# Optimization experiments

Hardware: AMD Instinct MI355X
Metric: run time of the kernel (lower is better)

Reference implementation:

```python
import jax, jax.numpy as jnp
import numpy as np

B, N = 8192, 200  # batch of patches, fixed 200 points per patch


def setup_inputs() -> dict:
    key = jax.random.key(0)
    k1, = jax.random.split(key, 1)
    network_in = jax.random.normal(k1, (B, N, 13), dtype=jnp.float32)
    # learned parameters per build(): outward_shift init 0.25, a init 1, b init 0
    outward_shift = jnp.full((1,), 0.25, dtype=jnp.float32)
    a = jnp.ones((1,), dtype=jnp.float32)
    b = jnp.zeros((1,), dtype=jnp.float32)
    return {"network_in": network_in, "outward_shift": outward_shift, "a": a, "b": b}


def reference(network_in, outward_shift, a, b):
    w = network_in[:, :, 0:1]          # [B,N,1]
    xyz1 = network_in[:, :, 1:4]
    xyz2 = network_in[:, :, 4:7]       # also orig_xyz2
    norm1 = network_in[:, :, 7:10]
    norm2 = network_in[:, :, 10:13]

    w = jax.nn.relu(a * w + b) + 1e-8  # [B,N,1]

    v1 = xyz1 + norm1 * outward_shift
    v2 = xyz2 + norm2 * outward_shift

    w_sum = jnp.sum(w, axis=1)                       # [B,1]
    v1_ctr = jnp.sum(v1 * w, axis=1) / w_sum         # [B,3]
    v2_ctr = jnp.sum(v2 * w, axis=1) / w_sum         # [B,3]
    v1 = v1 - v1_ctr[:, None, :]
    v2 = v2 - v2_ctr[:, None, :]

    # cov = v2^T diag(w) v1, done without materializing the NxN diagonal
    cov = jnp.einsum('bni,bn,bnj->bij', v2, w[:, :, 0], v1)  # [B,3,3]

    # tf.linalg.svd: cov = u diag(s) v^T  ->  jnp svd: cov = u diag(s) vh, v = vh^T
    u, s, vh = jnp.linalg.svd(cov)
    v = jnp.swapaxes(vh, -1, -2)

    VUt = jnp.einsum('bik,bjk->bij', v, u)           # v @ u^T
    det_VUt = jnp.linalg.det(VUt)                    # [B]
    ones = jnp.ones_like(det_VUt)
    d = jnp.stack([ones, ones, det_VUt], axis=-1)    # [B,3]

    # R = v @ diag([1,1,det]) @ u^T
    R = jnp.einsum('bik,bk,bjk->bij', v, d, u)       # [B,3,3]

    t = v1_ctr - jnp.einsum('bij,bj->bi', R, v2_ctr) # [B,3]
    new_coords = jnp.einsum('bij,bnj->bni', R, xyz2) + t[:, None, :]
    return new_coords
```

## Files before the change

### kernel.cpp

```cpp
#include <hip/hip_runtime.h>
#include <math.h>

#define NPTS 200
#define NCH  13
#define BLK  256
#define FPB  (NPTS * NCH)

typedef float f4u __attribute__((ext_vector_type(4), aligned(4)));

typedef struct { float x, y, z; } f3s;

#define ACCUMULATE(Q0,Q1,Q2,Q3,Q4,Q5,Q6,Q7,Q8,Q9,Q10,Q11,Q12)               \
    {                                                                        \
        float wt = aa * (Q0) + bb;                                           \
        wt = fmaxf(wt, 0.f) + 1e-8f;                                         \
        const float v1x = fmaf(shift, (Q7),  (Q1));                          \
        const float v1y = fmaf(shift, (Q8),  (Q2));                          \
        const float v1z = fmaf(shift, (Q9),  (Q3));                          \
        const float v2x = fmaf(shift, (Q10), (Q4));                          \
        const float v2y = fmaf(shift, (Q11), (Q5));                          \
        const float v2z = fmaf(shift, (Q12), (Q6));                          \
        const float wv2x = wt * v2x, wv2y = wt * v2y, wv2z = wt * v2z;       \
        acc[0] += wt;                                                        \
        acc[1] += wt * v1x; acc[2] += wt * v1y; acc[3] += wt * v1z;          \
        acc[4] += wv2x;     acc[5] += wv2y;     acc[6] += wv2z;              \
        acc[7]  += wv2x * v1x; acc[8]  += wv2x * v1y; acc[9]  += wv2x * v1z; \
        acc[10] += wv2y * v1x; acc[11] += wv2y * v1y; acc[12] += wv2y * v1z; \
        acc[13] += wv2z * v1x; acc[14] += wv2z * v1y; acc[15] += wv2z * v1z; \
    }

__global__ __launch_bounds__(BLK, 4) void fused_kernel(
    const float* __restrict__ net_in,
    const float* __restrict__ shift_p,
    const float* __restrict__ a_p,
    const float* __restrict__ b_p,
    float* __restrict__ out)
{
    const int tid = threadIdx.x;
    const int w   = tid >> 6;
    const int l   = tid & 63;
    const int b   = blockIdx.x * 4 + w;

    const float shift = shift_p[0];
    const float aa    = a_p[0];
    const float bb    = b_p[0];

    const float* src = net_in + (size_t)b * FPB;

    float acc[16];
    #pragma unroll
    for (int k = 0; k < 16; ++k) acc[k] = 0.f;

    float sx2[4], sy2[4], sz2[4];

    #pragma unroll
    for (int j = 0; j < 4; ++j) {
        if (j < 3 || l < 8) {
            const float* q = src + (l + 64 * j) * NCH;
            const f4u v0 = *(const f4u*)(q);
            const f4u v1 = *(const f4u*)(q + 4);
            const f4u v2 = *(const f4u*)(q + 8);
            const float q12 = q[12];
            ACCUMULATE(v0.x, v0.y, v0.z, v0.w,
                       v1.x, v1.y, v1.z, v1.w,
                       v2.x, v2.y, v2.z, v2.w, q12)
            sx2[j] = v1.x; sy2[j] = v1.y; sz2[j] = v1.z;
        } else {
            sx2[j] = 0.f; sy2[j] = 0.f; sz2[j] = 0.f;
        }
    }

    #pragma unroll
    for (int k = 0; k < 16; ++k) {
        acc[k] += __shfl_xor(acc[k], 32, 64);
        acc[k] += __shfl_xor(acc[k], 16, 64);
        acc[k] += __shfl_xor(acc[k],  8, 64);
        acc[k] += __shfl_xor(acc[k],  4, 64);
        acc[k] += __shfl_xor(acc[k],  2, 64);
        acc[k] += __shfl_xor(acc[k],  1, 64);
    }

    const float W = acc[0];
    const float invW = __builtin_amdgcn_rcpf(W);
    const float v1cx = acc[1] * invW, v1cy = acc[2] * invW, v1cz = acc[3] * invW;
    const float v2cx = acc[4] * invW, v2cy = acc[5] * invW, v2cz = acc[6] * invW;

    const float Sxx = acc[7]  - W * v2cx * v1cx;
    const float Sxy = acc[8]  - W * v2cx * v1cy;
    const float Sxz = acc[9]  - W * v2cx * v1cz;
    const float Syx = acc[10] - W * v2cy * v1cx;
    const float Syy = acc[11] - W * v2cy * v1cy;
    const float Syz = acc[12] - W * v2cy * v1cz;
    const float Szx = acc[13] - W * v2cz * v1cx;
    const float Szy = acc[14] - W * v2cz * v1cy;
    const float Szz = acc[15] - W * v2cz * v1cz;

    float Am[4][4];
    Am[0][0] = Sxx + Syy + Szz;
    Am[0][1] = Syz - Szy;  Am[0][2] = Szx - Sxz;  Am[0][3] = Sxy - Syx;
    Am[1][1] = Sxx - Syy - Szz;
    Am[1][2] = Sxy + Syx;  Am[1][3] = Szx + Sxz;
    Am[2][2] = -Sxx + Syy - Szz;
    Am[2][3] = Syz + Szy;
    Am[3][3] = -Sxx - Syy + Szz;
    Am[1][0] = Am[0][1]; Am[2][0] = Am[0][2]; Am[3][0] = Am[0][3];
    Am[2][1] = Am[1][2]; Am[3][1] = Am[1][3]; Am[3][2] = Am[2][3];

    float Vm[4][4] = {{1,0,0,0},{0,1,0,0},{0,0,1,0},{0,0,0,1}};

    const int prs[6][2] = {{0,1},{0,2},{0,3},{1,2},{1,3},{2,3}};
    for (int sweep = 0; sweep < 5; ++sweep) {
        #pragma unroll
        for (int r = 0; r < 6; ++r) {
            const int p = prs[r][0], q = prs[r][1];
            float apq = Am[p][q];
            if (apq != 0.0f) {
                float tau = (Am[q][q] - Am[p][p]) * 0.5f *
                            __builtin_amdgcn_rcpf(apq);
                float t = copysignf(1.0f, tau) * __builtin_amdgcn_rcpf(
                            fabsf(tau) +
                            __builtin_amdgcn_sqrtf(fmaf(tau, tau, 1.0f)));
                float c = __builtin_amdgcn_rsqf(fmaf(t, t, 1.0f));
                float s = t * c;
                #pragma unroll
                for (int k = 0; k < 4; ++k) {
                    float a1 = Am[p][k], a2 = Am[q][k];
                    Am[p][k] = c * a1 - s * a2;
                    Am[q][k] = s * a1 + c * a2;
                }
                #pragma unroll
                for (int k = 0; k < 4; ++k) {
                    float a1 = Am[k][p], a2 = Am[k][q];
                    Am[k][p] = c * a1 - s * a2;
                    Am[k][q] = s * a1 + c * a2;
                }
                #pragma unroll
                for (int k = 0; k < 4; ++k) {
                    float a1 = Vm[k][p], a2 = Vm[k][q];
                    Vm[k][p] = c * a1 - s * a2;
                    Vm[k][q] = s * a1 + c * a2;
                }
            }
        }
    }

    float bd = Am[0][0];
    float q0 = Vm[0][0], qx = Vm[1][0], qy = Vm[2][0], qz = Vm[3][0];
    if (Am[1][1] > bd) { bd = Am[1][1]; q0 = Vm[0][1]; qx = Vm[1][1]; qy = Vm[2][1]; qz = Vm[3][1]; }
    if (Am[2][2] > bd) { bd = Am[2][2]; q0 = Vm[0][2]; qx = Vm[1][2]; qy = Vm[2][2]; qz = Vm[3][2]; }
    if (Am[3][3] > bd) { bd = Am[3][3]; q0 = Vm[0][3]; qx = Vm[1][3]; qy = Vm[2][3]; qz = Vm[3][3]; }

    const float qn = __builtin_amdgcn_rsqf(q0*q0 + qx*qx + qy*qy + qz*qz);
    q0 *= qn; qx *= qn; qy *= qn; qz *= qn;

    const float R00 = q0*q0 + qx*qx - qy*qy - qz*qz;
    const float R01 = 2.0f * (qx*qy - q0*qz);
    const float R02 = 2.0f * (qx*qz + q0*qy);
    const float R10 = 2.0f * (qx*qy + q0*qz);
    const float R11 = q0*q0 - qx*qx + qy*qy - qz*qz;
    const float R12 = 2.0f * (qy*qz - q0*qx);
    const float R20 = 2.0f * (qx*qz - q0*qy);
    const float R21 = 2.0f * (qy*qz + q0*qx);
    const float R22 = q0*q0 - qx*qx - qy*qy + qz*qz;

    const float tx = v1cx - (R00 * v2cx + R01 * v2cy + R02 * v2cz);
    const float ty = v1cy - (R10 * v2cx + R11 * v2cy + R12 * v2cz);
    const float tz = v1cz - (R20 * v2cx + R21 * v2cy + R22 * v2cz);

    float* ob = out + (size_t)b * (NPTS * 3);
    #pragma unroll
    for (int j = 0; j < 4; ++j) {
        if (j < 3 || l < 8) {
            const int p = l + 64 * j;
            const float X = sx2[j], Y = sy2[j], Z = sz2[j];
            f3s o3;
            o3.x = R00 * X + R01 * Y + R02 * Z + tx;
            o3.y = R10 * X + R11 * Y + R12 * Z + ty;
            o3.z = R20 * X + R21 * Y + R22 * Z + tz;
            *(f3s*)(ob + p * 3) = o3;
        }
    }
}

extern "C" void kernel_launch(void* const* d_in, const int* in_sizes, int n_in,
                              void* d_out, int out_size, void* d_ws, size_t ws_size,
                              hipStream_t stream) {
    const float* net_in  = (const float*)d_in[0];
    const float* shift_p = (const float*)d_in[1];
    const float* a_p     = (const float*)d_in[2];
    const float* b_p     = (const float*)d_in[3];
    float* out = (float*)d_out;

    const int B = in_sizes[0] / FPB;
    (void)d_ws; (void)ws_size; (void)n_in; (void)out_size;

    fused_kernel<<<B / 4, BLK, 0, stream>>>(net_in, shift_p, a_p, b_p, out);
}
```

Baseline: 154.4 us.

## Process two patches per wavefront and streamline the 4x4 Jacobi eigen-solver

Each 64-lane wavefront now handles two batches (32 lanes each) instead of one. This halves the grid, drops one shuffle-reduction stage, and spreads the per-batch serial eigen-solve over more useful lanes. The Jacobi solver is rewritten to track only the diagonal and upper off-diagonal scalars, with closed-form diagonal updates and zeroed pivots. It uses predication instead of branches and runs 4 sweeps instead of 5. Each lane now holds more loads and registers (7 points), and the closed-form update plus fewer sweeps could slightly change accuracy.

```diff
diff --git a/kernel.cpp b/kernel.cpp
--- a/kernel.cpp
+++ b/kernel.cpp
@@ -29,6 +29,31 @@
         acc[13] += wv2z * v1x; acc[14] += wv2z * v1y; acc[15] += wv2z * v1z; \
     }
 
+#define ROTB(dp, dq, opq, e1p, e1q, e2p, e2q, P, Q)                          \
+    {                                                                        \
+        const float apq = opq;                                               \
+        const float tau = (dq - dp) * 0.5f * __builtin_amdgcn_rcpf(apq);     \
+        float tt = copysignf(1.0f, tau) * __builtin_amdgcn_rcpf(             \
+                     fabsf(tau) +                                            \
+                     __builtin_amdgcn_sqrtf(fmaf(tau, tau, 1.0f)));          \
+        tt = (apq != 0.0f) ? tt : 0.0f;                                      \
+        const float c = __builtin_amdgcn_rsqf(fmaf(tt, tt, 1.0f));           \
+        const float s = tt * c;                                              \
+        dp -= tt * apq;                                                      \
+        dq += tt * apq;                                                      \
+        opq = 0.0f;                                                          \
+        { const float t1 = e1p; e1p = c * t1 - s * e1q;                      \
+          e1q = s * t1 + c * e1q; }                                          \
+        { const float t2 = e2p; e2p = c * t2 - s * e2q;                      \
+          e2q = s * t2 + c * e2q; }                                          \
+        _Pragma("unroll")                                                    \
+        for (int k = 0; k < 4; ++k) {                                        \
+            const float a1 = Vm[k][P], a2 = Vm[k][Q];                        \
+            Vm[k][P] = c * a1 - s * a2;                                      \
+            Vm[k][Q] = s * a1 + c * a2;                                      \
+        }                                                                    \
+    }
+
 __global__ __launch_bounds__(BLK, 4) void fused_kernel(
     const float* __restrict__ net_in,
     const float* __restrict__ shift_p,
@@ -39,7 +64,8 @@
     const int tid = threadIdx.x;
     const int w   = tid >> 6;
     const int l   = tid & 63;
-    const int b   = blockIdx.x * 4 + w;
+    const int t   = l & 31;
+    const int b   = (blockIdx.x * 4 + w) * 2 + (l >> 5);
 
     const float shift = shift_p[0];
     const float aa    = a_p[0];
@@ -51,12 +77,12 @@
     #pragma unroll
     for (int k = 0; k < 16; ++k) acc[k] = 0.f;
 
-    float sx2[4], sy2[4], sz2[4];
-
-    #pragma unroll
-    for (int j = 0; j < 4; ++j) {
-        if (j < 3 || l < 8) {
-            const float* q = src + (l + 64 * j) * NCH;
+    float sx2[7], sy2[7], sz2[7];
+
+    #pragma unroll
+    for (int i = 0; i < 7; ++i) {
+        if (i < 6 || t < 8) {
+            const float* q = src + (t + 32 * i) * NCH;
             const f4u v0 = *(const f4u*)(q);
             const f4u v1 = *(const f4u*)(q + 4);
             const f4u v2 = *(const f4u*)(q + 8);
@@ -64,15 +90,14 @@
             ACCUMULATE(v0.x, v0.y, v0.z, v0.w,
                        v1.x, v1.y, v1.z, v1.w,
                        v2.x, v2.y, v2.z, v2.w, q12)
-            sx2[j] = v1.x; sy2[j] = v1.y; sz2[j] = v1.z;
+            sx2[i] = v1.x; sy2[i] = v1.y; sz2[i] = v1.z;
         } else {
-            sx2[j] = 0.f; sy2[j] = 0.f; sz2[j] = 0.f;
+            sx2[i] = 0.f; sy2[i] = 0.f; sz2[i] = 0.f;
         }
     }
 
     #pragma unroll
     for (int k = 0; k < 16; ++k) {
-        acc[k] += __shfl_xor(acc[k], 32, 64);
         acc[k] += __shfl_xor(acc[k], 16, 64);
         acc[k] += __shfl_xor(acc[k],  8, 64);
         acc[k] += __shfl_xor(acc[k],  4, 64);
@@ -95,60 +120,41 @@
     const float Szy = acc[14] - W * v2cz * v1cy;
     const float Szz = acc[15] - W * v2cz * v1cz;
 
-    float Am[4][4];
-    Am[0][0] = Sxx + Syy + Szz;
-    Am[0][1] = Syz - Szy;  Am[0][2] = Szx - Sxz;  Am[0][3] = Sxy - Syx;
-    Am[1][1] = Sxx - Syy - Szz;
-    Am[1][2] = Sxy + Syx;  Am[1][3] = Szx + Sxz;
-    Am[2][2] = -Sxx + Syy - Szz;
-    Am[2][3] = Syz + Szy;
-    Am[3][3] = -Sxx - Syy + Szz;
-    Am[1][0] = Am[0][1]; Am[2][0] = Am[0][2]; Am[3][0] = Am[0][3];
-    Am[2][1] = Am[1][2]; Am[3][1] = Am[1][3]; Am[3][2] = Am[2][3];
+    float d0  = Sxx + Syy + Szz;
+    float o01 = Syz - Szy;
+    float o02 = Szx - Sxz;
+    float o03 = Sxy - Syx;
+    float d1  = Sxx - Syy - Szz;
+    float o12 = Sxy + Syx;
+    float o13 = Szx + Sxz;
+    float d2  = -Sxx + Syy - Szz;
+    float o23 = Syz + Szy;
+    float d3  = -Sxx - Syy + Szz;
 
     float Vm[4][4] = {{1,0,0,0},{0,1,0,0},{0,0,1,0},{0,0,0,1}};
 
-    const int prs[6][2] = {{0,1},{0,2},{0,3},{1,2},{1,3},{2,3}};
-    for (int sweep = 0; sweep < 5; ++sweep) {
-        #pragma unroll
-        for (int r = 0; r < 6; ++r) {
-            const int p = prs[r][0], q = prs[r][1];
-            float apq = Am[p][q];
-            if (apq != 0.0f) {
-                float tau = (Am[q][q] - Am[p][p]) * 0.5f *
-                            __builtin_amdgcn_rcpf(apq);
-                float t = copysignf(1.0f, tau) * __builtin_amdgcn_rcpf(
-                            fabsf(tau) +
-                            __builtin_amdgcn_sqrtf(fmaf(tau, tau, 1.0f)));
-                float c = __builtin_amdgcn_rsqf(fmaf(t, t, 1.0f));
-                float s = t * c;
-                #pragma unroll
-                for (int k = 0; k < 4; ++k) {
-                    float a1 = Am[p][k], a2 = Am[q][k];
-                    Am[p][k] = c * a1 - s * a2;
-                    Am[q][k] = s * a1 + c * a2;
-                }
-                #pragma unroll
-                for (int k = 0; k < 4; ++k) {
-                    float a1 = Am[k][p], a2 = Am[k][q];
-                    Am[k][p] = c * a1 - s * a2;
-                    Am[k][q] = s * a1 + c * a2;
-                }
-                #pragma unroll
-                for (int k = 0; k < 4; ++k) {
-                    float a1 = Vm[k][p], a2 = Vm[k][q];
-                    Vm[k][p] = c * a1 - s * a2;
-                    Vm[k][q] = s * a1 + c * a2;
-                }
-            }
-        }
-    }
-
-    float bd = Am[0][0];
+    for (int sweep = 0; sweep < 4; ++sweep) {
+        ROTB(d0, d1, o01,  o02, o12,  o03, o13,  0, 1)
+        ROTB(d0, d2, o02,  o01, o12,  o03, o23,  0, 2)
+        ROTB(d0, d3, o03,  o01, o13,  o02, o23,  0, 3)
+        ROTB(d1, d2, o12,  o01, o02,  o13, o23,  1, 2)
+        ROTB(d1, d3, o13,  o01, o03,  o12, o23,  1, 3)
+        ROTB(d2, d3, o23,  o02, o03,  o12, o13,  2, 3)
+    }
+
+    float bd = d0;
     float q0 = Vm[0][0], qx = Vm[1][0], qy = Vm[2][0], qz = Vm[3][0];
-    if (Am[1][1] > bd) { bd = Am[1][1]; q0 = Vm[0][1]; qx = Vm[1][1]; qy = Vm[2][1]; qz = Vm[3][1]; }
-    if (Am[2][2] > bd) { bd = Am[2][2]; q0 = Vm[0][2]; qx = Vm[1][2]; qy = Vm[2][2]; qz = Vm[3][2]; }
-    if (Am[3][3] > bd) { bd = Am[3][3]; q0 = Vm[0][3]; qx = Vm[1][3]; qy = Vm[2][3]; qz = Vm[3][3]; }
+    { const bool c1 = d1 > bd;
+      bd = c1 ? d1 : bd;
+      q0 = c1 ? Vm[0][1] : q0; qx = c1 ? Vm[1][1] : qx;
+      qy = c1 ? Vm[2][1] : qy; qz = c1 ? Vm[3][1] : qz; }
+    { const bool c2 = d2 > bd;
+      bd = c2 ? d2 : bd;
+      q0 = c2 ? Vm[0][2] : q0; qx = c2 ? Vm[1][2] : qx;
+      qy = c2 ? Vm[2][2] : qy; qz = c2 ? Vm[3][2] : qz; }
+    { const bool c3 = d3 > bd;
+      q0 = c3 ? Vm[0][3] : q0; qx = c3 ? Vm[1][3] : qx;
+      qy = c3 ? Vm[2][3] : qy; qz = c3 ? Vm[3][3] : qz; }
 
     const float qn = __builtin_amdgcn_rsqf(q0*q0 + qx*qx + qy*qy + qz*qz);
     q0 *= qn; qx *= qn; qy *= qn; qz *= qn;
@@ -169,10 +175,10 @@
 
     float* ob = out + (size_t)b * (NPTS * 3);
     #pragma unroll
-    for (int j = 0; j < 4; ++j) {
-        if (j < 3 || l < 8) {
-            const int p = l + 64 * j;
-            const float X = sx2[j], Y = sy2[j], Z = sz2[j];
+    for (int i = 0; i < 7; ++i) {
+        if (i < 6 || t < 8) {
+            const int p = t + 32 * i;
+            const float X = sx2[i], Y = sy2[i], Z = sz2[i];
             f3s o3;
             o3.x = R00 * X + R01 * Y + R02 * Z + tx;
             o3.y = R10 * X + R11 * Y + R12 * Z + ty;
@@ -194,5 +200,5 @@
     const int B = in_sizes[0] / FPB;
     (void)d_ws; (void)ws_size; (void)n_in; (void)out_size;
 
-    fused_kernel<<<B / 4, BLK, 0, stream>>>(net_in, shift_p, a_p, b_p, out);
+    fused_kernel<<<B / 8, BLK, 0, stream>>>(net_in, shift_p, a_p, b_p, out);
 }
```

New measurement: 137.1 us. 11.2% less time.
